# Performance work log

Measured on AMD Instinct MI355X. Metric: run time of the kernel, lower is better.

The kernel has to match this reference:

```python
import jax, jax.numpy as jnp
import numpy as np

N_NODES = 50000
N_EDGES = 800000
IN_DIM = 128
HID = 32
HEADS = 4
EMB = 64
NEG_SLOPE = 0.2
LN_EPS = 1e-5


def setup_inputs() -> dict:
    key = jax.random.key(0)
    ks = jax.random.split(key, 16)
    s = 0.1
    inp = {
        'x': jax.random.normal(ks[0], (N_NODES, IN_DIM), dtype=jnp.float32),
        'edge_index': jax.random.randint(ks[1], (2, N_EDGES), 0, N_NODES, dtype=jnp.int64),
        # GATConv 1: in=128 -> heads=4, out_per_head=32, concat -> 128
        'W1': jax.random.normal(ks[2], (IN_DIM, HEADS * HID), dtype=jnp.float32) * s,
        'att_src1': jax.random.normal(ks[3], (HEADS, HID), dtype=jnp.float32) * s,
        'att_dst1': jax.random.normal(ks[4], (HEADS, HID), dtype=jnp.float32) * s,
        'b1': jnp.zeros((HEADS * HID,), dtype=jnp.float32),
        'gamma1': jnp.ones((HEADS * HID,), dtype=jnp.float32),
        'beta1': jnp.zeros((HEADS * HID,), dtype=jnp.float32),
        # GATConv 2: in=128 -> heads=1, out=64, concat=False
        'W2': jax.random.normal(ks[5], (HEADS * HID, EMB), dtype=jnp.float32) * s,
        'att_src2': jax.random.normal(ks[6], (1, EMB), dtype=jnp.float32) * s,
        'att_dst2': jax.random.normal(ks[7], (1, EMB), dtype=jnp.float32) * s,
        'b2': jnp.zeros((EMB,), dtype=jnp.float32),
        'gamma2': jnp.ones((EMB,), dtype=jnp.float32),
        'beta2': jnp.zeros((EMB,), dtype=jnp.float32),
    }
    return inp


def _gat_conv(x, src, dst, W, att_src, att_dst):
    # x: [N, F_in]; src/dst: [E'] (self loops included); W: [F_in, H*C]
    N = x.shape[0]
    H, C = att_src.shape
    h = (x @ W).reshape(N, H, C)                          # [N, H, C]
    a_s = jnp.sum(h * att_src, axis=-1)                   # [N, H]
    a_d = jnp.sum(h * att_dst, axis=-1)                   # [N, H]
    e = jax.nn.leaky_relu(a_s[src] + a_d[dst], NEG_SLOPE) # [E', H]
    # segment softmax over destination-node neighborhoods
    m = jax.ops.segment_max(e, dst, num_segments=N)       # [N, H]
    ex = jnp.exp(e - m[dst])
    den = jax.ops.segment_sum(ex, dst, num_segments=N)    # [N, H]
    alpha = ex / den[dst]                                  # [E', H]
    msg = h[src] * alpha[:, :, None]                       # [E', H, C]
    return jax.ops.segment_sum(msg, dst, num_segments=N)  # [N, H, C]


def _layer_norm(x, gamma, beta):
    mu = jnp.mean(x, axis=-1, keepdims=True)
    var = jnp.var(x, axis=-1, keepdims=True)
    return (x - mu) * jax.lax.rsqrt(var + LN_EPS) * gamma + beta


def reference(x, edge_index, W1, att_src1, att_dst1, b1, gamma1, beta1,
              W2, att_src2, att_dst2, b2, gamma2, beta2):
    N = x.shape[0]
    loops = jnp.arange(N, dtype=edge_index.dtype)
    src = jnp.concatenate([edge_index[0], loops])  # PyG add_self_loops=True
    dst = jnp.concatenate([edge_index[1], loops])

    # gat1: heads=4, concat=True
    h1 = _gat_conv(x, src, dst, W1, att_src1, att_dst1)   # [N, 4, 32]
    h1 = h1.reshape(N, -1) + b1                            # [N, 128]
    h1 = jax.nn.relu(_layer_norm(h1, gamma1, beta1))
    # dropout is identity in eval mode

    # gat2: heads=1, concat=False (mean over the single head)
    h2 = _gat_conv(h1, src, dst, W2, att_src2, att_dst2)  # [N, 1, 64]
    h2 = h2.mean(axis=1) + b2                              # [N, 64]
    return _layer_norm(h2, gamma2, beta2)
```

## Files before the change

kernel.cpp:

```cpp
#include <hip/hip_runtime.h>
#include <hip/hip_bf16.h>
#include <math.h>

#define N_NODES 50000
#define N_EDGES 800000
#define HEADS 4
#define HID 32
#define D1 128
#define D2 64
#define NEG_SLOPE 0.2f
#define LN_EPS 1e-5f

#define NB_SCAN ((N_NODES + 255) / 256)
#define CAP 64
#define GB1 ((N_NODES + 127) / 128)
#define DEGB 784

__device__ __forceinline__ float lrelu(float x) { return x > 0.f ? x : NEG_SLOPE * x; }
__device__ __forceinline__ float bf2f(__hip_bfloat16 v) { return __bfloat162float(v); }

__global__ __launch_bounds__(256) void gemm1_att1_degree_kernel(
    const float* __restrict__ X, const float* __restrict__ W,
    __hip_bfloat16* __restrict__ Y,
    const float* __restrict__ att_src, const float* __restrict__ att_dst,
    float* __restrict__ a_s, float* __restrict__ a_d,
    const int* __restrict__ dst, int* __restrict__ deg, int* __restrict__ rank) {
    if (blockIdx.x >= GB1) {
        int t0 = (blockIdx.x - GB1) * 256 + threadIdx.x;
        const int stride = DEGB * 256;
#pragma unroll
        for (int u = 0; u < 4; ++u) {
            int i = t0 + u * stride;
            if (i < N_EDGES) rank[i] = atomicAdd(&deg[dst[i]], 1);
        }
        return;
    }
    constexpr int COLS = 128;
    constexpr int CG = 8, RPT = 4;
    __shared__ float Wlds[128 * COLS];
    for (int i = threadIdx.x; i < 128 * COLS; i += 256) Wlds[i] = W[i];
    __syncthreads();

    int cg = threadIdx.x % CG;
    int rg = threadIdx.x / CG;
    int r0 = blockIdx.x * 128 + rg * RPT;
    int c0 = cg * 16;

    float acc[RPT][16];
#pragma unroll
    for (int i = 0; i < RPT; ++i)
#pragma unroll
        for (int j = 0; j < 16; ++j) acc[i][j] = 0.f;

    const float* xrow[RPT];
#pragma unroll
    for (int i = 0; i < RPT; ++i) {
        int ri = r0 + i;
        if (ri >= N_NODES) ri = N_NODES - 1;
        xrow[i] = X + (size_t)ri * 128;
    }

    for (int k = 0; k < 128; k += 4) {
        float4 xv[RPT];
#pragma unroll
        for (int i = 0; i < RPT; ++i) xv[i] = *(const float4*)&xrow[i][k];
#pragma unroll
        for (int kk = 0; kk < 4; ++kk) {
            const float* wrow = &Wlds[(k + kk) * COLS + c0];
            const float4 w0 = *(const float4*)(wrow + 0);
            const float4 w1 = *(const float4*)(wrow + 4);
            const float4 w2 = *(const float4*)(wrow + 8);
            const float4 w3 = *(const float4*)(wrow + 12);
#pragma unroll
            for (int i = 0; i < RPT; ++i) {
                float xk = (kk == 0) ? xv[i].x : (kk == 1) ? xv[i].y : (kk == 2) ? xv[i].z : xv[i].w;
                acc[i][0]  += xk * w0.x; acc[i][1]  += xk * w0.y;
                acc[i][2]  += xk * w0.z; acc[i][3]  += xk * w0.w;
                acc[i][4]  += xk * w1.x; acc[i][5]  += xk * w1.y;
                acc[i][6]  += xk * w1.z; acc[i][7]  += xk * w1.w;
                acc[i][8]  += xk * w2.x; acc[i][9]  += xk * w2.y;
                acc[i][10] += xk * w2.z; acc[i][11] += xk * w2.w;
                acc[i][12] += xk * w3.x; acc[i][13] += xk * w3.y;
                acc[i][14] += xk * w3.z; acc[i][15] += xk * w3.w;
            }
        }
    }

    int head = cg >> 1;
    int half = cg & 1;
    float asv[16], adv[16];
#pragma unroll
    for (int j = 0; j < 16; ++j) {
        asv[j] = att_src[head * 32 + half * 16 + j];
        adv[j] = att_dst[head * 32 + half * 16 + j];
    }
#pragma unroll
    for (int i = 0; i < RPT; ++i) {
        int r = r0 + i;
        float ps = 0.f, pd = 0.f;
#pragma unroll
        for (int j = 0; j < 16; ++j) {
            ps += acc[i][j] * asv[j];
            pd += acc[i][j] * adv[j];
        }
        ps += __shfl_xor(ps, 1, 64);
        pd += __shfl_xor(pd, 1, 64);
        if (r < N_NODES) {
            __hip_bfloat162* yp = (__hip_bfloat162*)(Y + (size_t)r * COLS + c0);
#pragma unroll
            for (int j = 0; j < 8; ++j) {
                __hip_bfloat162 p;
                p.x = __float2bfloat16(acc[i][2 * j]);
                p.y = __float2bfloat16(acc[i][2 * j + 1]);
                yp[j] = p;
            }
            if (half == 0) {
                a_s[r * 4 + head] = ps;
                a_d[r * 4 + head] = pd;
            }
        }
    }
}

__global__ __launch_bounds__(256) void scan1_kernel(const int* __restrict__ deg,
                                                    int* __restrict__ rpl,
                                                    int* __restrict__ bsum) {
    int i = blockIdx.x * 256 + threadIdx.x;
    int v = (i < N_NODES) ? deg[i] : 0;
    int lane = threadIdx.x & 63;
    int w = threadIdx.x >> 6;
    int x = v;
#pragma unroll
    for (int off = 1; off < 64; off <<= 1) {
        int t = __shfl_up(x, off, 64);
        if (lane >= off) x += t;
    }
    __shared__ int wsum[4];
    if (lane == 63) wsum[w] = x;
    __syncthreads();
    int wo = 0;
    if (w > 0) wo += wsum[0];
    if (w > 1) wo += wsum[1];
    if (w > 2) wo += wsum[2];
    if (i <= N_NODES) rpl[i] = x - v + wo;
    if (threadIdx.x == 255) bsum[blockIdx.x] = x + wo;
}

__global__ __launch_bounds__(256) void scan2_kernel(const int* __restrict__ bsum,
                                                    int* __restrict__ boff) {
    int i = threadIdx.x;
    int v = (i < NB_SCAN) ? bsum[i] : 0;
    int lane = threadIdx.x & 63;
    int w = threadIdx.x >> 6;
    int x = v;
#pragma unroll
    for (int off = 1; off < 64; off <<= 1) {
        int t = __shfl_up(x, off, 64);
        if (lane >= off) x += t;
    }
    __shared__ int wsum[4];
    if (lane == 63) wsum[w] = x;
    __syncthreads();
    int wo = 0;
    if (w > 0) wo += wsum[0];
    if (w > 1) wo += wsum[1];
    if (w > 2) wo += wsum[2];
    if (i < NB_SCAN) boff[i] = x - v + wo;
}

__global__ __launch_bounds__(256) void scatter_kernel(const int* __restrict__ src,
                                                      const int* __restrict__ dst,
                                                      const int* __restrict__ rpl,
                                                      const int* __restrict__ boff,
                                                      const int* __restrict__ rank,
                                                      int* __restrict__ col) {
    int i = blockIdx.x * blockDim.x + threadIdx.x;
    if (i < N_EDGES) {
        int d = dst[i];
        int pos = rpl[d] + boff[d >> 8] + rank[i];
        col[pos] = src[i];
    }
}

__global__ __launch_bounds__(256) void agg1_kernel(const __hip_bfloat16* __restrict__ h,
                                                   const float* __restrict__ a_s,
                                                   const float* __restrict__ a_d,
                                                   const int* __restrict__ rpl,
                                                   const int* __restrict__ boff,
                                                   const int* __restrict__ col,
                                                   const float* __restrict__ b1,
                                                   const float* __restrict__ gamma,
                                                   const float* __restrict__ beta,
                                                   float* __restrict__ out) {
    __shared__ int colsh[4][CAP];
    __shared__ float wsh[4][CAP * 4];
    int wv = threadIdx.x >> 6;
    int lane = threadIdx.x & 63;
    int n = blockIdx.x * 4 + wv;
    int nn = (n < N_NODES) ? n : N_NODES - 1;
    int head = lane >> 4;
    int c = 2 * lane;

    const float4 ad4 = *(const float4*)&a_d[nn * 4];
    int beg = rpl[nn] + boff[nn >> 8];
    int end = rpl[nn + 1] + boff[(nn + 1) >> 8];
    int deg = end - beg;

    float den0 = 0.f, den1 = 0.f, den2 = 0.f, den3 = 0.f;
    for (int t = lane; t < deg; t += 64) {
        int s = col[beg + t];
        const float4 as4 = *(const float4*)&a_s[s * 4];
        float w0 = __expf(lrelu(as4.x + ad4.x));
        float w1 = __expf(lrelu(as4.y + ad4.y));
        float w2 = __expf(lrelu(as4.z + ad4.z));
        float w3 = __expf(lrelu(as4.w + ad4.w));
        if (t < CAP) {
            colsh[wv][t] = s;
            *(float4*)&wsh[wv][t * 4] = make_float4(w0, w1, w2, w3);
        }
        den0 += w0; den1 += w1; den2 += w2; den3 += w3;
    }
#pragma unroll
    for (int m = 1; m < 64; m <<= 1) {
        den0 += __shfl_xor(den0, m, 64);
        den1 += __shfl_xor(den1, m, 64);
        den2 += __shfl_xor(den2, m, 64);
        den3 += __shfl_xor(den3, m, 64);
    }
    float adh = (head == 0) ? ad4.x : (head == 1) ? ad4.y : (head == 2) ? ad4.z : ad4.w;
    float wself = __expf(lrelu(a_s[nn * 4 + head] + adh));
    float den = ((head == 0) ? den0 : (head == 1) ? den1 : (head == 2) ? den2 : den3) + wself;

    __syncthreads();

    float ax0 = 0.f, ay0 = 0.f, ax1 = 0.f, ay1 = 0.f;
    int m0 = (deg < CAP) ? deg : CAP;
    int j = 0;
    for (; j + 3 < m0; j += 4) {
        int s0 = colsh[wv][j + 0], s1 = colsh[wv][j + 1];
        int s2 = colsh[wv][j + 2], s3 = colsh[wv][j + 3];
        float w0 = wsh[wv][(j + 0) * 4 + head], w1 = wsh[wv][(j + 1) * 4 + head];
        float w2 = wsh[wv][(j + 2) * 4 + head], w3 = wsh[wv][(j + 3) * 4 + head];
        __hip_bfloat162 h0 = ((const __hip_bfloat162*)h)[(size_t)s0 * 64 + lane];
        __hip_bfloat162 h1 = ((const __hip_bfloat162*)h)[(size_t)s1 * 64 + lane];
        __hip_bfloat162 h2v = ((const __hip_bfloat162*)h)[(size_t)s2 * 64 + lane];
        __hip_bfloat162 h3 = ((const __hip_bfloat162*)h)[(size_t)s3 * 64 + lane];
        ax0 += w0 * bf2f(h0.x); ay0 += w0 * bf2f(h0.y);
        ax1 += w1 * bf2f(h1.x); ay1 += w1 * bf2f(h1.y);
        ax0 += w2 * bf2f(h2v.x); ay0 += w2 * bf2f(h2v.y);
        ax1 += w3 * bf2f(h3.x); ay1 += w3 * bf2f(h3.y);
    }
    for (; j < m0; ++j) {
        int s = colsh[wv][j];
        float w = wsh[wv][j * 4 + head];
        __hip_bfloat162 hv = ((const __hip_bfloat162*)h)[(size_t)s * 64 + lane];
        ax0 += w * bf2f(hv.x); ay0 += w * bf2f(hv.y);
    }
    for (; j < deg; ++j) {
        int s = col[beg + j];
        float w = __expf(lrelu(a_s[s * 4 + head] + adh));
        __hip_bfloat162 hv = ((const __hip_bfloat162*)h)[(size_t)s * 64 + lane];
        ax0 += w * bf2f(hv.x); ay0 += w * bf2f(hv.y);
    }
    {
        __hip_bfloat162 hv = ((const __hip_bfloat162*)h)[(size_t)nn * 64 + lane];
        ax0 += wself * bf2f(hv.x); ay0 += wself * bf2f(hv.y);
    }
    float inv = 1.f / den;
    float vx = (ax0 + ax1) * inv + b1[c];
    float vy = (ay0 + ay1) * inv + b1[c + 1];

    float s1 = vx + vy, s2 = vx * vx + vy * vy;
#pragma unroll
    for (int m = 1; m < 64; m <<= 1) {
        s1 += __shfl_xor(s1, m, 64);
        s2 += __shfl_xor(s2, m, 64);
    }
    float mean = s1 * (1.f / 128.f);
    float var = s2 * (1.f / 128.f) - mean * mean;
    float r = rsqrtf(var + LN_EPS);
    float ox = fmaxf(0.f, (vx - mean) * r * gamma[c] + beta[c]);
    float oy = fmaxf(0.f, (vy - mean) * r * gamma[c + 1] + beta[c + 1]);
    if (n < N_NODES) *(float2*)&out[(size_t)n * 128 + c] = make_float2(ox, oy);
}

__global__ __launch_bounds__(256) void gemm2_att2_kernel(const float* __restrict__ X,
                                                         const float* __restrict__ W,
                                                         __hip_bfloat16* __restrict__ Y,
                                                         const float* __restrict__ att_src,
                                                         const float* __restrict__ att_dst,
                                                         float* __restrict__ a_s,
                                                         float* __restrict__ a_d) {
    constexpr int COLS = 64;
    constexpr int CG = 4, RPT = 2;
    __shared__ float Wlds[128 * COLS];
    for (int i = threadIdx.x; i < 128 * COLS; i += 256) Wlds[i] = W[i];
    __syncthreads();

    int cg = threadIdx.x % CG;
    int rg = threadIdx.x / CG;
    int r0 = blockIdx.x * 128 + rg * RPT;
    int c0 = cg * 16;

    float acc[RPT][16];
#pragma unroll
    for (int i = 0; i < RPT; ++i)
#pragma unroll
        for (int j = 0; j < 16; ++j) acc[i][j] = 0.f;

    const float* xrow[RPT];
#pragma unroll
    for (int i = 0; i < RPT; ++i) {
        int ri = r0 + i;
        if (ri >= N_NODES) ri = N_NODES - 1;
        xrow[i] = X + (size_t)ri * 128;
    }

    for (int k = 0; k < 128; k += 4) {
        float4 xv[RPT];
#pragma unroll
        for (int i = 0; i < RPT; ++i) xv[i] = *(const float4*)&xrow[i][k];
#pragma unroll
        for (int kk = 0; kk < 4; ++kk) {
            const float* wrow = &Wlds[(k + kk) * COLS + c0];
            const float4 w0 = *(const float4*)(wrow + 0);
            const float4 w1 = *(const float4*)(wrow + 4);
            const float4 w2 = *(const float4*)(wrow + 8);
            const float4 w3 = *(const float4*)(wrow + 12);
#pragma unroll
            for (int i = 0; i < RPT; ++i) {
                float xk = (kk == 0) ? xv[i].x : (kk == 1) ? xv[i].y : (kk == 2) ? xv[i].z : xv[i].w;
                acc[i][0]  += xk * w0.x; acc[i][1]  += xk * w0.y;
                acc[i][2]  += xk * w0.z; acc[i][3]  += xk * w0.w;
                acc[i][4]  += xk * w1.x; acc[i][5]  += xk * w1.y;
                acc[i][6]  += xk * w1.z; acc[i][7]  += xk * w1.w;
                acc[i][8]  += xk * w2.x; acc[i][9]  += xk * w2.y;
                acc[i][10] += xk * w2.z; acc[i][11] += xk * w2.w;
                acc[i][12] += xk * w3.x; acc[i][13] += xk * w3.y;
                acc[i][14] += xk * w3.z; acc[i][15] += xk * w3.w;
            }
        }
    }

    float asv[16], adv[16];
#pragma unroll
    for (int j = 0; j < 16; ++j) {
        asv[j] = att_src[c0 + j];
        adv[j] = att_dst[c0 + j];
    }
#pragma unroll
    for (int i = 0; i < RPT; ++i) {
        int r = r0 + i;
        float ps = 0.f, pd = 0.f;
#pragma unroll
        for (int j = 0; j < 16; ++j) {
            ps += acc[i][j] * asv[j];
            pd += acc[i][j] * adv[j];
        }
        ps += __shfl_xor(ps, 1, 64);
        pd += __shfl_xor(pd, 1, 64);
        ps += __shfl_xor(ps, 2, 64);
        pd += __shfl_xor(pd, 2, 64);
        if (r < N_NODES) {
            __hip_bfloat162* yp = (__hip_bfloat162*)(Y + (size_t)r * COLS + c0);
#pragma unroll
            for (int j = 0; j < 8; ++j) {
                __hip_bfloat162 p;
                p.x = __float2bfloat16(acc[i][2 * j]);
                p.y = __float2bfloat16(acc[i][2 * j + 1]);
                yp[j] = p;
            }
            if (cg == 0) {
                a_s[r] = ps;
                a_d[r] = pd;
            }
        }
    }
}

__global__ __launch_bounds__(256) void agg2_kernel(const __hip_bfloat16* __restrict__ h,
                                                   const float* __restrict__ a_s,
                                                   const float* __restrict__ a_d,
                                                   const int* __restrict__ rpl,
                                                   const int* __restrict__ boff,
                                                   const int* __restrict__ col,
                                                   const float* __restrict__ b2,
                                                   const float* __restrict__ gamma,
                                                   const float* __restrict__ beta,
                                                   float* __restrict__ out) {
    __shared__ int colsh[4][CAP];
    __shared__ float wsh[4][CAP];
    int wv = threadIdx.x >> 6;
    int lane = threadIdx.x & 63;
    int n = blockIdx.x * 4 + wv;
    int nn = (n < N_NODES) ? n : N_NODES - 1;

    float adh = a_d[nn];
    int beg = rpl[nn] + boff[nn >> 8];
    int end = rpl[nn + 1] + boff[(nn + 1) >> 8];
    int deg = end - beg;

    float den = 0.f;
    for (int t = lane; t < deg; t += 64) {
        int s = col[beg + t];
        float w = __expf(lrelu(a_s[s] + adh));
        if (t < CAP) {
            colsh[wv][t] = s;
            wsh[wv][t] = w;
        }
        den += w;
    }
#pragma unroll
    for (int m = 1; m < 64; m <<= 1) den += __shfl_xor(den, m, 64);
    float wself = __expf(lrelu(a_s[nn] + adh));
    den += wself;

    __syncthreads();

    float a0 = 0.f, a1 = 0.f;
    int m0 = (deg < CAP) ? deg : CAP;
    int j = 0;
    for (; j + 3 < m0; j += 4) {
        int s0 = colsh[wv][j + 0], s1 = colsh[wv][j + 1];
        int s2 = colsh[wv][j + 2], s3 = colsh[wv][j + 3];
        float w0 = wsh[wv][j + 0], w1 = wsh[wv][j + 1];
        float w2 = wsh[wv][j + 2], w3 = wsh[wv][j + 3];
        a0 += w0 * bf2f(h[(size_t)s0 * 64 + lane]);
        a1 += w1 * bf2f(h[(size_t)s1 * 64 + lane]);
        a0 += w2 * bf2f(h[(size_t)s2 * 64 + lane]);
        a1 += w3 * bf2f(h[(size_t)s3 * 64 + lane]);
    }
    for (; j < m0; ++j) {
        a0 += wsh[wv][j] * bf2f(h[(size_t)colsh[wv][j] * 64 + lane]);
    }
    for (; j < deg; ++j) {
        int s = col[beg + j];
        float w = __expf(lrelu(a_s[s] + adh));
        a0 += w * bf2f(h[(size_t)s * 64 + lane]);
    }
    a0 += wself * bf2f(h[(size_t)nn * 64 + lane]);

    float v = (a0 + a1) / den + b2[lane];

    float s1 = v, s2 = v * v;
#pragma unroll
    for (int m = 1; m < 64; m <<= 1) {
        s1 += __shfl_xor(s1, m, 64);
        s2 += __shfl_xor(s2, m, 64);
    }
    float mean = s1 * (1.f / 64.f);
    float var = s2 * (1.f / 64.f) - mean * mean;
    float r = rsqrtf(var + LN_EPS);
    if (n < N_NODES) out[(size_t)n * 64 + lane] = (v - mean) * r * gamma[lane] + beta[lane];
}

extern "C" void kernel_launch(void* const* d_in, const int* in_sizes, int n_in,
                              void* d_out, int out_size, void* d_ws, size_t ws_size,
                              hipStream_t stream) {
    const float* x        = (const float*)d_in[0];
    const int*   ei       = (const int*)d_in[1];
    const float* W1       = (const float*)d_in[2];
    const float* att_src1 = (const float*)d_in[3];
    const float* att_dst1 = (const float*)d_in[4];
    const float* b1       = (const float*)d_in[5];
    const float* gamma1   = (const float*)d_in[6];
    const float* beta1    = (const float*)d_in[7];
    const float* W2       = (const float*)d_in[8];
    const float* att_src2 = (const float*)d_in[9];
    const float* att_dst2 = (const float*)d_in[10];
    const float* b2       = (const float*)d_in[11];
    const float* gamma2   = (const float*)d_in[12];
    const float* beta2    = (const float*)d_in[13];
    const int* src = ei;
    const int* dst = ei + N_EDGES;
    float* out = (float*)d_out;

    char* ws = (char*)d_ws;
    size_t off = 0;
    auto alloc = [&](size_t bytes) -> void* {
        void* p = ws + off;
        off += bytes;
        off = (off + 255) & ~(size_t)255;
        return p;
    };
    __hip_bfloat16* h1pre = (__hip_bfloat16*)alloc((size_t)N_NODES * 128 * 2);
    __hip_bfloat16* h2pre = (__hip_bfloat16*)alloc((size_t)N_NODES * 64 * 2);
    float* a_s1   = (float*)alloc((size_t)N_NODES * 4 * 4);
    float* a_d1   = (float*)alloc((size_t)N_NODES * 4 * 4);
    float* h1n    = (float*)alloc((size_t)N_NODES * 128 * 4);
    float* a_s2   = (float*)alloc((size_t)N_NODES * 4);
    float* a_d2   = (float*)alloc((size_t)N_NODES * 4);
    int* deg      = (int*)alloc((size_t)N_NODES * 4);
    int* rpl      = (int*)alloc((size_t)(N_NODES + 1) * 4);
    int* col      = (int*)alloc((size_t)N_EDGES * 4);
    int* rank     = (int*)alloc((size_t)N_EDGES * 4);
    int* bsum     = (int*)alloc((size_t)NB_SCAN * 4);
    int* boff     = (int*)alloc((size_t)NB_SCAN * 4);

    hipMemsetAsync(deg, 0, (size_t)N_NODES * 4, stream);

    const int EB = (N_EDGES + 255) / 256;
    const int NWB = (N_NODES + 3) / 4;

    gemm1_att1_degree_kernel<<<GB1 + DEGB, 256, 0, stream>>>(
        x, W1, h1pre, att_src1, att_dst1, a_s1, a_d1, dst, deg, rank);
    scan1_kernel<<<NB_SCAN, 256, 0, stream>>>(deg, rpl, bsum);
    scan2_kernel<<<1, 256, 0, stream>>>(bsum, boff);
    scatter_kernel<<<EB, 256, 0, stream>>>(src, dst, rpl, boff, rank, col);

    agg1_kernel<<<NWB, 256, 0, stream>>>(h1pre, a_s1, a_d1, rpl, boff, col, b1, gamma1, beta1, h1n);

    gemm2_att2_kernel<<<(N_NODES + 127) / 128, 256, 0, stream>>>(
        h1n, W2, h2pre, att_src2, att_dst2, a_s2, a_d2);
    agg2_kernel<<<NWB, 256, 0, stream>>>(h2pre, a_s2, a_d2, rpl, boff, col, b2, gamma2, beta2, out);
}
```

Measured before the change: 251.7 us.

## Tile weight matrix in K-chunks and remap threads for LDS broadcast in GEMM kernels

Both GEMM kernels now stage the weight matrix in K-slices (32 rows for gemm1, 64 for gemm2) instead of holding the full 64KB/32KB in shared memory. This cuts LDS use per block and should allow more resident blocks. Threads are also remapped so a wavefront shares one column group, which makes the LDS weight reads broadcasts. In gemm2 the attention-score reduction now goes through shared memory because the column groups sit in different waves. The cost is extra barriers per K-chunk and possibly less coalesced X row loads.

```diff
diff --git a/kernel.cpp b/kernel.cpp
--- a/kernel.cpp
+++ b/kernel.cpp
@@ -25,6 +25,7 @@
     const float* __restrict__ att_src, const float* __restrict__ att_dst,
     float* __restrict__ a_s, float* __restrict__ a_d,
     const int* __restrict__ dst, int* __restrict__ deg, int* __restrict__ rank) {
+    __shared__ float Wlds[32 * 128];
     if (blockIdx.x >= GB1) {
         int t0 = (blockIdx.x - GB1) * 256 + threadIdx.x;
         const int stride = DEGB * 256;
@@ -35,59 +36,64 @@
         }
         return;
     }
-    constexpr int COLS = 128;
-    constexpr int CG = 8, RPT = 4;
-    __shared__ float Wlds[128 * COLS];
-    for (int i = threadIdx.x; i < 128 * COLS; i += 256) Wlds[i] = W[i];
-    __syncthreads();
-
-    int cg = threadIdx.x % CG;
-    int rg = threadIdx.x / CG;
-    int r0 = blockIdx.x * 128 + rg * RPT;
+    int tid = threadIdx.x;
+    int cg = tid >> 5;
+    int rg = tid & 31;
     int c0 = cg * 16;
-
-    float acc[RPT][16];
-#pragma unroll
-    for (int i = 0; i < RPT; ++i)
+    int head = cg >> 1;
+    int half = cg & 1;
+    int r0 = blockIdx.x * 128 + rg * 4;
+
+    float acc[4][16];
+#pragma unroll
+    for (int i = 0; i < 4; ++i)
 #pragma unroll
         for (int j = 0; j < 16; ++j) acc[i][j] = 0.f;
 
-    const float* xrow[RPT];
-#pragma unroll
-    for (int i = 0; i < RPT; ++i) {
+    const float* xrow[4];
+#pragma unroll
+    for (int i = 0; i < 4; ++i) {
         int ri = r0 + i;
         if (ri >= N_NODES) ri = N_NODES - 1;
         xrow[i] = X + (size_t)ri * 128;
     }
 
-    for (int k = 0; k < 128; k += 4) {
-        float4 xv[RPT];
-#pragma unroll
-        for (int i = 0; i < RPT; ++i) xv[i] = *(const float4*)&xrow[i][k];
-#pragma unroll
-        for (int kk = 0; kk < 4; ++kk) {
-            const float* wrow = &Wlds[(k + kk) * COLS + c0];
-            const float4 w0 = *(const float4*)(wrow + 0);
-            const float4 w1 = *(const float4*)(wrow + 4);
-            const float4 w2 = *(const float4*)(wrow + 8);
-            const float4 w3 = *(const float4*)(wrow + 12);
-#pragma unroll
-            for (int i = 0; i < RPT; ++i) {
-                float xk = (kk == 0) ? xv[i].x : (kk == 1) ? xv[i].y : (kk == 2) ? xv[i].z : xv[i].w;
-                acc[i][0]  += xk * w0.x; acc[i][1]  += xk * w0.y;
-                acc[i][2]  += xk * w0.z; acc[i][3]  += xk * w0.w;
-                acc[i][4]  += xk * w1.x; acc[i][5]  += xk * w1.y;
-                acc[i][6]  += xk * w1.z; acc[i][7]  += xk * w1.w;
-                acc[i][8]  += xk * w2.x; acc[i][9]  += xk * w2.y;
-                acc[i][10] += xk * w2.z; acc[i][11] += xk * w2.w;
-                acc[i][12] += xk * w3.x; acc[i][13] += xk * w3.y;
-                acc[i][14] += xk * w3.z; acc[i][15] += xk * w3.w;
+    for (int kb = 0; kb < 128; kb += 32) {
+        {
+            const float4* s = (const float4*)(W + (size_t)kb * 128) + tid * 4;
+            float4* d = (float4*)&Wlds[tid * 16];
+            d[0] = s[0]; d[1] = s[1]; d[2] = s[2]; d[3] = s[3];
+        }
+        __syncthreads();
+#pragma unroll
+        for (int k = 0; k < 32; k += 4) {
+            float4 xv[4];
+#pragma unroll
+            for (int i = 0; i < 4; ++i) xv[i] = *(const float4*)&xrow[i][kb + k];
+#pragma unroll
+            for (int kk = 0; kk < 4; ++kk) {
+                const float* wrow = &Wlds[(k + kk) * 128 + c0];
+                const float4 w0 = *(const float4*)(wrow + 0);
+                const float4 w1 = *(const float4*)(wrow + 4);
+                const float4 w2 = *(const float4*)(wrow + 8);
+                const float4 w3 = *(const float4*)(wrow + 12);
+#pragma unroll
+                for (int i = 0; i < 4; ++i) {
+                    float xk = (kk == 0) ? xv[i].x : (kk == 1) ? xv[i].y : (kk == 2) ? xv[i].z : xv[i].w;
+                    acc[i][0]  += xk * w0.x; acc[i][1]  += xk * w0.y;
+                    acc[i][2]  += xk * w0.z; acc[i][3]  += xk * w0.w;
+                    acc[i][4]  += xk * w1.x; acc[i][5]  += xk * w1.y;
+                    acc[i][6]  += xk * w1.z; acc[i][7]  += xk * w1.w;
+                    acc[i][8]  += xk * w2.x; acc[i][9]  += xk * w2.y;
+                    acc[i][10] += xk * w2.z; acc[i][11] += xk * w2.w;
+                    acc[i][12] += xk * w3.x; acc[i][13] += xk * w3.y;
+                    acc[i][14] += xk * w3.z; acc[i][15] += xk * w3.w;
+                }
             }
         }
-    }
-
-    int head = cg >> 1;
-    int half = cg & 1;
+        __syncthreads();
+    }
+
     float asv[16], adv[16];
 #pragma unroll
     for (int j = 0; j < 16; ++j) {
@@ -95,7 +101,7 @@
         adv[j] = att_dst[head * 32 + half * 16 + j];
     }
 #pragma unroll
-    for (int i = 0; i < RPT; ++i) {
+    for (int i = 0; i < 4; ++i) {
         int r = r0 + i;
         float ps = 0.f, pd = 0.f;
 #pragma unroll
@@ -103,10 +109,10 @@
             ps += acc[i][j] * asv[j];
             pd += acc[i][j] * adv[j];
         }
-        ps += __shfl_xor(ps, 1, 64);
-        pd += __shfl_xor(pd, 1, 64);
+        ps += __shfl_xor(ps, 32, 64);
+        pd += __shfl_xor(pd, 32, 64);
         if (r < N_NODES) {
-            __hip_bfloat162* yp = (__hip_bfloat162*)(Y + (size_t)r * COLS + c0);
+            __hip_bfloat162* yp = (__hip_bfloat162*)(Y + (size_t)r * 128 + c0);
 #pragma unroll
             for (int j = 0; j < 8; ++j) {
                 __hip_bfloat162 p;
@@ -291,78 +297,68 @@
                                                          const float* __restrict__ att_dst,
                                                          float* __restrict__ a_s,
                                                          float* __restrict__ a_d) {
-    constexpr int COLS = 64;
-    constexpr int CG = 4, RPT = 2;
-    __shared__ float Wlds[128 * COLS];
-    for (int i = threadIdx.x; i < 128 * COLS; i += 256) Wlds[i] = W[i];
-    __syncthreads();
-
-    int cg = threadIdx.x % CG;
-    int rg = threadIdx.x / CG;
-    int r0 = blockIdx.x * 128 + rg * RPT;
+    __shared__ float Wlds[64 * 64];
+    int tid = threadIdx.x;
+    int cg = tid >> 6;
+    int rg = tid & 63;
     int c0 = cg * 16;
-
-    float acc[RPT][16];
-#pragma unroll
-    for (int i = 0; i < RPT; ++i)
+    int r0 = blockIdx.x * 128 + rg * 2;
+
+    float acc[2][16];
+#pragma unroll
+    for (int i = 0; i < 2; ++i)
 #pragma unroll
         for (int j = 0; j < 16; ++j) acc[i][j] = 0.f;
 
-    const float* xrow[RPT];
-#pragma unroll
-    for (int i = 0; i < RPT; ++i) {
+    const float* xrow[2];
+#pragma unroll
+    for (int i = 0; i < 2; ++i) {
         int ri = r0 + i;
         if (ri >= N_NODES) ri = N_NODES - 1;
         xrow[i] = X + (size_t)ri * 128;
     }
 
-    for (int k = 0; k < 128; k += 4) {
-        float4 xv[RPT];
-#pragma unroll
-        for (int i = 0; i < RPT; ++i) xv[i] = *(const float4*)&xrow[i][k];
-#pragma unroll
-        for (int kk = 0; kk < 4; ++kk) {
-            const float* wrow = &Wlds[(k + kk) * COLS + c0];
-            const float4 w0 = *(const float4*)(wrow + 0);
-            const float4 w1 = *(const float4*)(wrow + 4);
-            const float4 w2 = *(const float4*)(wrow + 8);
-            const float4 w3 = *(const float4*)(wrow + 12);
-#pragma unroll
-            for (int i = 0; i < RPT; ++i) {
-                float xk = (kk == 0) ? xv[i].x : (kk == 1) ? xv[i].y : (kk == 2) ? xv[i].z : xv[i].w;
-                acc[i][0]  += xk * w0.x; acc[i][1]  += xk * w0.y;
-                acc[i][2]  += xk * w0.z; acc[i][3]  += xk * w0.w;
-                acc[i][4]  += xk * w1.x; acc[i][5]  += xk * w1.y;
-                acc[i][6]  += xk * w1.z; acc[i][7]  += xk * w1.w;
-                acc[i][8]  += xk * w2.x; acc[i][9]  += xk * w2.y;
-                acc[i][10] += xk * w2.z; acc[i][11] += xk * w2.w;
-                acc[i][12] += xk * w3.x; acc[i][13] += xk * w3.y;
-                acc[i][14] += xk * w3.z; acc[i][15] += xk * w3.w;
+    for (int kb = 0; kb < 128; kb += 64) {
+        {
+            const float4* s = (const float4*)(W + (size_t)kb * 64) + tid * 4;
+            float4* d = (float4*)&Wlds[tid * 16];
+            d[0] = s[0]; d[1] = s[1]; d[2] = s[2]; d[3] = s[3];
+        }
+        __syncthreads();
+#pragma unroll
+        for (int k = 0; k < 64; k += 4) {
+            float4 xv[2];
+#pragma unroll
+            for (int i = 0; i < 2; ++i) xv[i] = *(const float4*)&xrow[i][kb + k];
+#pragma unroll
+            for (int kk = 0; kk < 4; ++kk) {
+                const float* wrow = &Wlds[(k + kk) * 64 + c0];
+                const float4 w0 = *(const float4*)(wrow + 0);
+                const float4 w1 = *(const float4*)(wrow + 4);
+                const float4 w2 = *(const float4*)(wrow + 8);
+                const float4 w3 = *(const float4*)(wrow + 12);
+#pragma unroll
+                for (int i = 0; i < 2; ++i) {
+                    float xk = (kk == 0) ? xv[i].x : (kk == 1) ? xv[i].y : (kk == 2) ? xv[i].z : xv[i].w;
+                    acc[i][0]  += xk * w0.x; acc[i][1]  += xk * w0.y;
+                    acc[i][2]  += xk * w0.z; acc[i][3]  += xk * w0.w;
+                    acc[i][4]  += xk * w1.x; acc[i][5]  += xk * w1.y;
+                    acc[i][6]  += xk * w1.z; acc[i][7]  += xk * w1.w;
+                    acc[i][8]  += xk * w2.x; acc[i][9]  += xk * w2.y;
+                    acc[i][10] += xk * w2.z; acc[i][11] += xk * w2.w;
+                    acc[i][12] += xk * w3.x; acc[i][13] += xk * w3.y;
+                    acc[i][14] += xk * w3.z; acc[i][15] += xk * w3.w;
+                }
             }
         }
-    }
-
-    float asv[16], adv[16];
-#pragma unroll
-    for (int j = 0; j < 16; ++j) {
-        asv[j] = att_src[c0 + j];
-        adv[j] = att_dst[c0 + j];
-    }
-#pragma unroll
-    for (int i = 0; i < RPT; ++i) {
+        __syncthreads();
+    }
+
+#pragma unroll
+    for (int i = 0; i < 2; ++i) {
         int r = r0 + i;
-        float ps = 0.f, pd = 0.f;
-#pragma unroll
-        for (int j = 0; j < 16; ++j) {
-            ps += acc[i][j] * asv[j];
-            pd += acc[i][j] * adv[j];
-        }
-        ps += __shfl_xor(ps, 1, 64);
-        pd += __shfl_xor(pd, 1, 64);
-        ps += __shfl_xor(ps, 2, 64);
-        pd += __shfl_xor(pd, 2, 64);
         if (r < N_NODES) {
-            __hip_bfloat162* yp = (__hip_bfloat162*)(Y + (size_t)r * COLS + c0);
+            __hip_bfloat162* yp = (__hip_bfloat162*)(Y + (size_t)r * 64 + c0);
 #pragma unroll
             for (int j = 0; j < 8; ++j) {
                 __hip_bfloat162 p;
@@ -370,10 +366,35 @@
                 p.y = __float2bfloat16(acc[i][2 * j + 1]);
                 yp[j] = p;
             }
-            if (cg == 0) {
-                a_s[r] = ps;
-                a_d[r] = pd;
-            }
+        }
+    }
+
+    float ps[2], pd[2];
+#pragma unroll
+    for (int i = 0; i < 2; ++i) {
+        ps[i] = 0.f; pd[i] = 0.f;
+#pragma unroll
+        for (int j = 0; j < 16; ++j) {
+            ps[i] += acc[i][j] * att_src[c0 + j];
+            pd[i] += acc[i][j] * att_dst[c0 + j];
+        }
+    }
+    float* red = Wlds;
+#pragma unroll
+    for (int i = 0; i < 2; ++i) {
+        int rr = rg * 2 + i;
+        red[rr * 4 + cg] = ps[i];
+        red[512 + rr * 4 + cg] = pd[i];
+    }
+    __syncthreads();
+    if (tid < 128) {
+        int r = blockIdx.x * 128 + tid;
+        float as = red[tid * 4 + 0] + red[tid * 4 + 1] + red[tid * 4 + 2] + red[tid * 4 + 3];
+        float ad = red[512 + tid * 4 + 0] + red[512 + tid * 4 + 1] +
+                   red[512 + tid * 4 + 2] + red[512 + tid * 4 + 3];
+        if (r < N_NODES) {
+            a_s[r] = as;
+            a_d[r] = ad;
         }
     }
 }
```

Result: slower. 277.7 us (+10.3%).
